# Optimization experiments

Measured on AMD Instinct MI355X. Metric: run time of the kernel, lower is better.

## Reference

```python
import jax, jax.numpy as jnp
import numpy as np

B, S, E, FFN, Q = 8, 2048, 512, 2048, 8


def setup_inputs() -> dict:
    key = jax.random.key(0)
    k0, k1, k2, k3 = jax.random.split(key, 4)
    x = jax.random.normal(k0, (B, S, E), dtype=jnp.float32)
    ry = jax.random.normal(k1, (Q,), dtype=jnp.float32)  # trainable RY angles
    w1 = jax.random.normal(k2, (FFN, Q), dtype=jnp.float32) / np.sqrt(Q).astype(np.float32)
    b1 = jnp.zeros((FFN,), dtype=jnp.float32)
    w2 = jax.random.normal(k3, (E, FFN), dtype=jnp.float32) / np.sqrt(FFN).astype(np.float32)
    b2 = jnp.zeros((E,), dtype=jnp.float32)
    return {"x": x, "ry": ry, "w1": w1, "b1": b1, "w2": w2, "b2": b2}


def reference(x, ry, w1, b1, w2, b2):
    # Quantum layer: each qubit i starts in |0>, gets RX(x[..., i]) then RY(ry[i]),
    # then PauliZ expectation. Product state => closed form <Z_i> = cos(x_i) * cos(ry_i).
    nq = ry.shape[0]
    z = jnp.cos(x[..., :nq]) * jnp.cos(ry)  # [B, S, Q]
    # dropout is identity in eval mode
    h = jnp.einsum("bsq,fq->bsf", z, w1) + b1  # fc1
    return jnp.einsum("bsf,ef->bse", jax.nn.relu(h), w2) + b2  # fc2
```

## Files before the change

kernel.cpp:

```cpp
#include <hip/hip_runtime.h>
#include <cstdint>
#include <cstddef>


typedef __attribute__((ext_vector_type(8))) short s16x8;
typedef __attribute__((ext_vector_type(4))) float f32x4;

__device__ __forceinline__ unsigned short f2bf(float f) {
  unsigned int u = __float_as_uint(f);
  unsigned int r = u + 0x7fffu + ((u >> 16) & 1u);
  return (unsigned short)(r >> 16);
}

__device__ __forceinline__ unsigned pk_bf16(float lo, float hi) {
  unsigned ul = __float_as_uint(lo) + 0x8000u;
  unsigned uh = __float_as_uint(hi) + 0x8000u;
  return __builtin_amdgcn_perm(uh, ul, 0x07060302u);
}

__global__ __launch_bounds__(256) void k_cvt(const float* __restrict__ w2,
                                             const float* __restrict__ w1,
                                             unsigned short* __restrict__ w2b,
                                             unsigned short* __restrict__ w1b) {
  const int bid = blockIdx.x;
  const float* src = (bid < 1024) ? w2 : w1;
  unsigned short* dst = (bid < 1024) ? w2b : w1b;
  const int b = (bid < 1024) ? bid : (bid - 1024);
  size_t i = ((size_t)b * 256 + threadIdx.x) * 4;
  float4 v = *(const float4*)(src + i);
  uint2 p;
  p.x = f2bf(v.x) | ((unsigned)f2bf(v.y) << 16);
  p.y = f2bf(v.z) | ((unsigned)f2bf(v.w) << 16);
  *(uint2*)(dst + i) = p;
}

__global__ __launch_bounds__(256) void k_fused(
    const float* __restrict__ x, const float* __restrict__ ry,
    const unsigned short* __restrict__ w1b,
    const unsigned short* __restrict__ w2b,
    const float* __restrict__ b2, float* __restrict__ out) {
  __shared__ unsigned short z_lds[128 * 8];
  __shared__ unsigned short As[128 * 40];

  const int t = threadIdx.x;
  const int lane = t & 63;
  const int w = t >> 6;
  const int fr = lane & 15;
  const int quad = lane >> 4;
  const int mt = blockIdx.x >> 2;
  const int nt = blockIdx.x & 3;
  const int r0 = mt * 128;
  const int c0 = nt * 128;

  {
    const int row = t >> 1, q4 = (t & 1) * 4;
    float4 xv = *(const float4*)(x + (size_t)(r0 + row) * 512 + q4);
    float c0r = __cosf(ry[q4 + 0]), c1r = __cosf(ry[q4 + 1]);
    float c2r = __cosf(ry[q4 + 2]), c3r = __cosf(ry[q4 + 3]);
    uint2 p;
    p.x = f2bf(__cosf(xv.x) * c0r) | ((unsigned)f2bf(__cosf(xv.y) * c1r) << 16);
    p.y = f2bf(__cosf(xv.z) * c2r) | ((unsigned)f2bf(__cosf(xv.w) * c3r) << 16);
    *(uint2*)(z_lds + row * 8 + q4) = p;
  }
  __syncthreads();

  s16x8 bz[2];
#pragma unroll
  for (int i = 0; i < 2; ++i) {
    s16x8 v = {0, 0, 0, 0, 0, 0, 0, 0};
    if (quad == 0) v = *(const s16x8*)(z_lds + ((2 * w + i) * 16 + fr) * 8);
    bz[i] = v;
  }

  const int wm = (w >> 1) * 64;
  const int wn = (w & 1) * 64;

  const unsigned short* gB[4];
#pragma unroll
  for (int j = 0; j < 4; ++j)
    gB[j] = w2b + (size_t)(c0 + wn + j * 16 + fr) * 2048 + quad * 8;
  const unsigned short* gW1 = w1b + fr * 8;

  f32x4 acc[4][4];
#pragma unroll
  for (int i = 0; i < 4; ++i)
#pragma unroll
    for (int j = 0; j < 4; ++j) acc[i][j] = (f32x4){0.f, 0.f, 0.f, 0.f};

  const f32x4 zero4 = (f32x4){0.f, 0.f, 0.f, 0.f};
  unsigned short* wrA0 = As + ((2 * w) * 16 + fr) * 40 + quad * 4;
  unsigned short* wrA1 = As + ((2 * w + 1) * 16 + fr) * 40 + quad * 4;
  const unsigned short* rdA = As + (wm + fr) * 40 + quad * 8;

  for (int kt = 0; kt < 64; ++kt) {
    s16x8 b2f[4];
#pragma unroll
    for (int j = 0; j < 4; ++j) b2f[j] = *(const s16x8*)gB[j];
#pragma unroll
    for (int j = 0; j < 4; ++j) gB[j] += 32;

    s16x8 aw0 = *(const s16x8*)gW1;
    s16x8 aw1 = *(const s16x8*)(gW1 + 128);
    gW1 += 256;

    f32x4 p00 = __builtin_amdgcn_mfma_f32_16x16x32_bf16(aw0, bz[0], zero4, 0, 0, 0);
    f32x4 p01 = __builtin_amdgcn_mfma_f32_16x16x32_bf16(aw0, bz[1], zero4, 0, 0, 0);
    f32x4 p10 = __builtin_amdgcn_mfma_f32_16x16x32_bf16(aw1, bz[0], zero4, 0, 0, 0);
    f32x4 p11 = __builtin_amdgcn_mfma_f32_16x16x32_bf16(aw1, bz[1], zero4, 0, 0, 0);

    uint2 q00, q01, q10, q11;
    q00.x = pk_bf16(fmaxf(p00[0], 0.f), fmaxf(p00[1], 0.f));
    q00.y = pk_bf16(fmaxf(p00[2], 0.f), fmaxf(p00[3], 0.f));
    q01.x = pk_bf16(fmaxf(p01[0], 0.f), fmaxf(p01[1], 0.f));
    q01.y = pk_bf16(fmaxf(p01[2], 0.f), fmaxf(p01[3], 0.f));
    q10.x = pk_bf16(fmaxf(p10[0], 0.f), fmaxf(p10[1], 0.f));
    q10.y = pk_bf16(fmaxf(p10[2], 0.f), fmaxf(p10[3], 0.f));
    q11.x = pk_bf16(fmaxf(p11[0], 0.f), fmaxf(p11[1], 0.f));
    q11.y = pk_bf16(fmaxf(p11[2], 0.f), fmaxf(p11[3], 0.f));
    *(uint2*)(wrA0) = q00;
    *(uint2*)(wrA1) = q01;
    *(uint2*)(wrA0 + 16) = q10;
    *(uint2*)(wrA1 + 16) = q11;

    __syncthreads();

    s16x8 a2[4];
#pragma unroll
    for (int i = 0; i < 4; ++i) a2[i] = *(const s16x8*)(rdA + i * 16 * 40);
#pragma unroll
    for (int i = 0; i < 4; ++i)
#pragma unroll
      for (int j = 0; j < 4; ++j)
        acc[i][j] = __builtin_amdgcn_mfma_f32_16x16x32_bf16(a2[i], b2f[j],
                                                            acc[i][j], 0, 0, 0);
    __syncthreads();
  }

  float bias[4];
#pragma unroll
  for (int j = 0; j < 4; ++j) bias[j] = b2[c0 + wn + j * 16 + fr];
#pragma unroll
  for (int i = 0; i < 4; ++i) {
    const int rbase = r0 + wm + i * 16 + quad * 4;
#pragma unroll
    for (int rr = 0; rr < 4; ++rr) {
      float* crow = out + (size_t)(rbase + rr) * 512;
#pragma unroll
      for (int j = 0; j < 4; ++j)
        crow[c0 + wn + j * 16 + fr] = acc[i][j][rr] + bias[j];
    }
  }
}

__global__ __launch_bounds__(256) void k_naive(
    const float* __restrict__ x, const float* __restrict__ ry,
    const float* __restrict__ w1, const float* __restrict__ b1,
    const float* __restrict__ w2, const float* __restrict__ b2,
    float* __restrict__ out) {
  __shared__ float zsh[8];
  __shared__ float acts[2048];
  const int r = blockIdx.x;
  const int t = threadIdx.x;
  if (t < 8) zsh[t] = __cosf(x[(size_t)r * 512 + t]) * __cosf(ry[t]);
  __syncthreads();
  float z[8];
#pragma unroll
  for (int q = 0; q < 8; ++q) z[q] = zsh[q];
#pragma unroll
  for (int i = 0; i < 8; ++i) {
    const int f = t * 8 + i;
    const float* wr = w1 + (size_t)f * 8;
    float4 a = *(const float4*)wr;
    float4 b = *(const float4*)(wr + 4);
    float h = b1[f] + z[0] * a.x + z[1] * a.y + z[2] * a.z + z[3] * a.w +
              z[4] * b.x + z[5] * b.y + z[6] * b.z + z[7] * b.w;
    acts[f] = fmaxf(h, 0.0f);
  }
  __syncthreads();
  for (int ee = 0; ee < 2; ++ee) {
    const int e = t + ee * 256;
    const float* wr = w2 + (size_t)e * 2048;
    float acc = b2[e];
    for (int f = 0; f < 2048; f += 4) {
      float4 wv = *(const float4*)(wr + f);
      float4 av = *(const float4*)(acts + f);
      acc += av.x * wv.x + av.y * wv.y + av.z * wv.z + av.w * wv.w;
    }
    out[(size_t)r * 512 + e] = acc;
  }
}

extern "C" void kernel_launch(void* const* d_in, const int* in_sizes, int n_in,
                              void* d_out, int out_size, void* d_ws,
                              size_t ws_size, hipStream_t stream) {
  const float* x  = (const float*)d_in[0];
  const float* ry = (const float*)d_in[1];
  const float* w1 = (const float*)d_in[2];
  const float* b1 = (const float*)d_in[3];
  const float* w2 = (const float*)d_in[4];
  const float* b2 = (const float*)d_in[5];
  float* out = (float*)d_out;

  const size_t w2b_bytes = (size_t)512 * 2048 * 2;
  const size_t need = w2b_bytes + (size_t)2048 * 8 * 2;

  if (ws_size < need) {
    k_naive<<<dim3(16384), dim3(256), 0, stream>>>(x, ry, w1, b1, w2, b2, out);
    return;
  }

  unsigned short* w2b = (unsigned short*)d_ws;
  unsigned short* w1b = (unsigned short*)((char*)d_ws + w2b_bytes);

  (void)b1;
  k_cvt<<<dim3(1040), dim3(256), 0, stream>>>(w2, w1, w2b, w1b);
  k_fused<<<dim3(512), dim3(256), 0, stream>>>(x, ry, w1b, w2b, b2, out);
  (void)in_sizes; (void)n_in; (void)out_size;
}
```

Baseline: 171.3 us.

## Compute fc1 activations in registers per wave, removing LDS staging and barriers

Each wave now produces its fc1 activations directly as the A operand of the fc2 MFMA through a permuted w1 row layout, eliminating the shared-memory round trip and both per-step barriers. The bias b1 is folded into the fc1 MFMA by padding K with a constant-one column. The next k step's activation fragment is computed ahead. The block tile shrinks to 64x128 with double the grid, which lowers w2 reuse per block and raises global/L2 load traffic.

```diff
diff --git a/kernel.cpp b/kernel.cpp
--- a/kernel.cpp
+++ b/kernel.cpp
@@ -18,30 +18,48 @@
   return __builtin_amdgcn_perm(uh, ul, 0x07060302u);
 }
 
+__device__ __forceinline__ s16x8 u4s(uint4 u) {
+  union { uint4 a; s16x8 b; } c; c.a = u; return c.b;
+}
+
 __global__ __launch_bounds__(256) void k_cvt(const float* __restrict__ w2,
                                              const float* __restrict__ w1,
+                                             const float* __restrict__ b1,
                                              unsigned short* __restrict__ w2b,
-                                             unsigned short* __restrict__ w1b) {
-  const int bid = blockIdx.x;
-  const float* src = (bid < 1024) ? w2 : w1;
-  unsigned short* dst = (bid < 1024) ? w2b : w1b;
-  const int b = (bid < 1024) ? bid : (bid - 1024);
-  size_t i = ((size_t)b * 256 + threadIdx.x) * 4;
-  float4 v = *(const float4*)(src + i);
-  uint2 p;
-  p.x = f2bf(v.x) | ((unsigned)f2bf(v.y) << 16);
-  p.y = f2bf(v.z) | ((unsigned)f2bf(v.w) << 16);
-  *(uint2*)(dst + i) = p;
+                                             unsigned short* __restrict__ w1x) {
+  const int bid = blockIdx.x, t = threadIdx.x;
+  if (bid < 1024) {
+    size_t i = ((size_t)bid * 256 + t) * 4;
+    float4 v = *(const float4*)(w2 + i);
+    uint2 p;
+    p.x = f2bf(v.x) | ((unsigned)f2bf(v.y) << 16);
+    p.y = f2bf(v.z) | ((unsigned)f2bf(v.w) << 16);
+    *(uint2*)(w2b + i) = p;
+  } else {
+    const int row = (bid - 1024) * 256 + t;
+    const float* wr = w1 + (size_t)row * 8;
+    float4 a = *(const float4*)wr;
+    float4 b = *(const float4*)(wr + 4);
+    uint4 s0;
+    s0.x = f2bf(a.x) | ((unsigned)f2bf(a.y) << 16);
+    s0.y = f2bf(a.z) | ((unsigned)f2bf(a.w) << 16);
+    s0.z = f2bf(b.x) | ((unsigned)f2bf(b.y) << 16);
+    s0.w = f2bf(b.z) | ((unsigned)f2bf(b.w) << 16);
+    uint4 s1 = {(unsigned)f2bf(b1[row]), 0u, 0u, 0u};
+    uint4 zz = {0u, 0u, 0u, 0u};
+    unsigned short* dst = w1x + (size_t)row * 32;
+    *(uint4*)dst = s0;
+    *(uint4*)(dst + 8) = s1;
+    *(uint4*)(dst + 16) = zz;
+    *(uint4*)(dst + 24) = zz;
+  }
 }
 
 __global__ __launch_bounds__(256) void k_fused(
     const float* __restrict__ x, const float* __restrict__ ry,
-    const unsigned short* __restrict__ w1b,
+    const unsigned short* __restrict__ w1x,
     const unsigned short* __restrict__ w2b,
     const float* __restrict__ b2, float* __restrict__ out) {
-  __shared__ unsigned short z_lds[128 * 8];
-  __shared__ unsigned short As[128 * 40];
-
   const int t = threadIdx.x;
   const int lane = t & 63;
   const int w = t >> 6;
@@ -49,106 +67,84 @@
   const int quad = lane >> 4;
   const int mt = blockIdx.x >> 2;
   const int nt = blockIdx.x & 3;
-  const int r0 = mt * 128;
+  const int r0 = mt * 64;
   const int c0 = nt * 128;
-
-  {
-    const int row = t >> 1, q4 = (t & 1) * 4;
-    float4 xv = *(const float4*)(x + (size_t)(r0 + row) * 512 + q4);
-    float c0r = __cosf(ry[q4 + 0]), c1r = __cosf(ry[q4 + 1]);
-    float c2r = __cosf(ry[q4 + 2]), c3r = __cosf(ry[q4 + 3]);
-    uint2 p;
-    p.x = f2bf(__cosf(xv.x) * c0r) | ((unsigned)f2bf(__cosf(xv.y) * c1r) << 16);
-    p.y = f2bf(__cosf(xv.z) * c2r) | ((unsigned)f2bf(__cosf(xv.w) * c3r) << 16);
-    *(uint2*)(z_lds + row * 8 + q4) = p;
-  }
-  __syncthreads();
-
-  s16x8 bz[2];
-#pragma unroll
-  for (int i = 0; i < 2; ++i) {
-    s16x8 v = {0, 0, 0, 0, 0, 0, 0, 0};
-    if (quad == 0) v = *(const s16x8*)(z_lds + ((2 * w + i) * 16 + fr) * 8);
-    bz[i] = v;
-  }
-
-  const int wm = (w >> 1) * 64;
-  const int wn = (w & 1) * 64;
-
-  const unsigned short* gB[4];
-#pragma unroll
-  for (int j = 0; j < 4; ++j)
-    gB[j] = w2b + (size_t)(c0 + wn + j * 16 + fr) * 2048 + quad * 8;
-  const unsigned short* gW1 = w1b + fr * 8;
-
-  f32x4 acc[4][4];
-#pragma unroll
-  for (int i = 0; i < 4; ++i)
-#pragma unroll
-    for (int j = 0; j < 4; ++j) acc[i][j] = (f32x4){0.f, 0.f, 0.f, 0.f};
+  const int m0 = r0 + w * 16;
+
+  const float* xr = x + (size_t)(m0 + fr) * 512;
+  float4 xa = *(const float4*)xr;
+  float4 xb = *(const float4*)(xr + 4);
+  float4 ra = *(const float4*)ry;
+  float4 rb = *(const float4*)(ry + 4);
+  unsigned zd0 = f2bf(__cosf(xa.x) * __cosf(ra.x)) |
+                 ((unsigned)f2bf(__cosf(xa.y) * __cosf(ra.y)) << 16);
+  unsigned zd1 = f2bf(__cosf(xa.z) * __cosf(ra.z)) |
+                 ((unsigned)f2bf(__cosf(xa.w) * __cosf(ra.w)) << 16);
+  unsigned zd2 = f2bf(__cosf(xb.x) * __cosf(rb.x)) |
+                 ((unsigned)f2bf(__cosf(xb.y) * __cosf(rb.y)) << 16);
+  unsigned zd3 = f2bf(__cosf(xb.z) * __cosf(rb.z)) |
+                 ((unsigned)f2bf(__cosf(xb.w) * __cosf(rb.w)) << 16);
+  uint4 bzu;
+  bzu.x = (quad == 0) ? zd0 : ((quad == 1) ? 0x00003F80u : 0u);
+  bzu.y = (quad == 0) ? zd1 : 0u;
+  bzu.z = (quad == 0) ? zd2 : 0u;
+  bzu.w = (quad == 0) ? zd3 : 0u;
+  const s16x8 bz = u4s(bzu);
+
+  const int rowp = 8 * (fr >> 2) + (fr & 3);
+  const unsigned short* gW = w1x + (size_t)rowp * 32 + quad * 8;
+
+  const unsigned short* gB[8];
+#pragma unroll
+  for (int j = 0; j < 8; ++j)
+    gB[j] = w2b + (size_t)(c0 + j * 16 + fr) * 2048 + quad * 8;
+
+  f32x4 acc[8];
+#pragma unroll
+  for (int j = 0; j < 8; ++j) acc[j] = (f32x4){0.f, 0.f, 0.f, 0.f};
 
   const f32x4 zero4 = (f32x4){0.f, 0.f, 0.f, 0.f};
-  unsigned short* wrA0 = As + ((2 * w) * 16 + fr) * 40 + quad * 4;
-  unsigned short* wrA1 = As + ((2 * w + 1) * 16 + fr) * 40 + quad * 4;
-  const unsigned short* rdA = As + (wm + fr) * 40 + quad * 8;
+
+#define MAKE_A(kt_, dst_)                                                     \
+  {                                                                           \
+    const unsigned short* p_ = gW + (size_t)(kt_)*1024;     \
+    s16x8 aw1_ = *(const s16x8*)p_;                                           \
+    s16x8 aw2_ = *(const s16x8*)(p_ + 128);                      \
+    f32x4 p1_ = __builtin_amdgcn_mfma_f32_16x16x32_bf16(aw1_, bz, zero4, 0, 0, 0); \
+    f32x4 p2_ = __builtin_amdgcn_mfma_f32_16x16x32_bf16(aw2_, bz, zero4, 0, 0, 0); \
+    uint4 u_;                                                                 \
+    u_.x = pk_bf16(fmaxf(p1_[0], 0.f), fmaxf(p1_[1], 0.f));                   \
+    u_.y = pk_bf16(fmaxf(p1_[2], 0.f), fmaxf(p1_[3], 0.f));                   \
+    u_.z = pk_bf16(fmaxf(p2_[0], 0.f), fmaxf(p2_[1], 0.f));                   \
+    u_.w = pk_bf16(fmaxf(p2_[2], 0.f), fmaxf(p2_[3], 0.f));                   \
+    dst_ = u4s(u_);                                                           \
+  }
+
+  s16x8 afrag;
+  MAKE_A(0, afrag);
 
   for (int kt = 0; kt < 64; ++kt) {
-    s16x8 b2f[4];
-#pragma unroll
-    for (int j = 0; j < 4; ++j) b2f[j] = *(const s16x8*)gB[j];
-#pragma unroll
-    for (int j = 0; j < 4; ++j) gB[j] += 32;
-
-    s16x8 aw0 = *(const s16x8*)gW1;
-    s16x8 aw1 = *(const s16x8*)(gW1 + 128);
-    gW1 += 256;
-
-    f32x4 p00 = __builtin_amdgcn_mfma_f32_16x16x32_bf16(aw0, bz[0], zero4, 0, 0, 0);
-    f32x4 p01 = __builtin_amdgcn_mfma_f32_16x16x32_bf16(aw0, bz[1], zero4, 0, 0, 0);
-    f32x4 p10 = __builtin_amdgcn_mfma_f32_16x16x32_bf16(aw1, bz[0], zero4, 0, 0, 0);
-    f32x4 p11 = __builtin_amdgcn_mfma_f32_16x16x32_bf16(aw1, bz[1], zero4, 0, 0, 0);
-
-    uint2 q00, q01, q10, q11;
-    q00.x = pk_bf16(fmaxf(p00[0], 0.f), fmaxf(p00[1], 0.f));
-    q00.y = pk_bf16(fmaxf(p00[2], 0.f), fmaxf(p00[3], 0.f));
-    q01.x = pk_bf16(fmaxf(p01[0], 0.f), fmaxf(p01[1], 0.f));
-    q01.y = pk_bf16(fmaxf(p01[2], 0.f), fmaxf(p01[3], 0.f));
-    q10.x = pk_bf16(fmaxf(p10[0], 0.f), fmaxf(p10[1], 0.f));
-    q10.y = pk_bf16(fmaxf(p10[2], 0.f), fmaxf(p10[3], 0.f));
-    q11.x = pk_bf16(fmaxf(p11[0], 0.f), fmaxf(p11[1], 0.f));
-    q11.y = pk_bf16(fmaxf(p11[2], 0.f), fmaxf(p11[3], 0.f));
-    *(uint2*)(wrA0) = q00;
-    *(uint2*)(wrA1) = q01;
-    *(uint2*)(wrA0 + 16) = q10;
-    *(uint2*)(wrA1 + 16) = q11;
-
-    __syncthreads();
-
-    s16x8 a2[4];
-#pragma unroll
-    for (int i = 0; i < 4; ++i) a2[i] = *(const s16x8*)(rdA + i * 16 * 40);
-#pragma unroll
-    for (int i = 0; i < 4; ++i)
-#pragma unroll
-      for (int j = 0; j < 4; ++j)
-        acc[i][j] = __builtin_amdgcn_mfma_f32_16x16x32_bf16(a2[i], b2f[j],
-                                                            acc[i][j], 0, 0, 0);
-    __syncthreads();
-  }
-
-  float bias[4];
-#pragma unroll
-  for (int j = 0; j < 4; ++j) bias[j] = b2[c0 + wn + j * 16 + fr];
-#pragma unroll
-  for (int i = 0; i < 4; ++i) {
-    const int rbase = r0 + wm + i * 16 + quad * 4;
-#pragma unroll
-    for (int rr = 0; rr < 4; ++rr) {
-      float* crow = out + (size_t)(rbase + rr) * 512;
-#pragma unroll
-      for (int j = 0; j < 4; ++j)
-        crow[c0 + wn + j * 16 + fr] = acc[i][j][rr] + bias[j];
-    }
+    s16x8 bf[8];
+#pragma unroll
+    for (int j = 0; j < 8; ++j) bf[j] = *(const s16x8*)(gB[j] + kt * 32);
+    const s16x8 acur = afrag;
+    if (kt < 63) MAKE_A(kt + 1, afrag);
+#pragma unroll
+    for (int j = 0; j < 8; ++j)
+      acc[j] = __builtin_amdgcn_mfma_f32_16x16x32_bf16(acur, bf[j], acc[j],
+                                                       0, 0, 0);
+  }
+#undef MAKE_A
+
+  float bias[8];
+#pragma unroll
+  for (int j = 0; j < 8; ++j) bias[j] = b2[c0 + j * 16 + fr];
+  const int mrow = m0 + quad * 4;
+#pragma unroll
+  for (int rr = 0; rr < 4; ++rr) {
+    float* orow = out + (size_t)(mrow + rr) * 512 + c0;
+#pragma unroll
+    for (int j = 0; j < 8; ++j) orow[j * 16 + fr] = acc[j][rr] + bias[j];
   }
 }
 
@@ -202,18 +198,16 @@
   float* out = (float*)d_out;
 
   const size_t w2b_bytes = (size_t)512 * 2048 * 2;
-  const size_t need = w2b_bytes + (size_t)2048 * 8 * 2;
-
-  if (ws_size < need) {
+  const size_t w1x_bytes = (size_t)2048 * 32 * 2;
+  if (ws_size < w2b_bytes + w1x_bytes) {
     k_naive<<<dim3(16384), dim3(256), 0, stream>>>(x, ry, w1, b1, w2, b2, out);
     return;
   }
 
   unsigned short* w2b = (unsigned short*)d_ws;
-  unsigned short* w1b = (unsigned short*)((char*)d_ws + w2b_bytes);
-
-  (void)b1;
-  k_cvt<<<dim3(1040), dim3(256), 0, stream>>>(w2, w1, w2b, w1b);
-  k_fused<<<dim3(512), dim3(256), 0, stream>>>(x, ry, w1b, w2b, b2, out);
+  unsigned short* w1x = (unsigned short*)((char*)d_ws + w2b_bytes);
+
+  k_cvt<<<dim3(1032), dim3(256), 0, stream>>>(w2, w1, b1, w2b, w1x);
+  k_fused<<<dim3(1024), dim3(256), 0, stream>>>(x, ry, w1x, w2b, b2, out);
   (void)in_sizes; (void)n_in; (void)out_size;
 }
```

Measured after the change: 343.9 us. +100.8%, slower.
